# Performance work log

Hardware: AMD Instinct MI355X
Metric: run time of the kernel (lower is better)

The kernel has to match this reference:

```python
import jax, jax.numpy as jnp
import numpy as np

MAX_COC = 50.0
NUM_PLANES = 32
KERNEL_CAP = 31
B, C, H, W = 4, 3, 512, 512


def _plane_kernels():
    """Static per-plane Gaussian kernels, mirroring the torch loop exactly."""
    planes = np.linspace(0.0, MAX_COC, NUM_PLANES)
    kernels = []
    for coc in planes:
        if coc < 0.5:
            kernels.append(None)  # identity (no blur)
            continue
        sigma = coc / 2.355
        k = int(2 * coc + 1)
        if k % 2 == 0:
            k += 1
        k = min(k, KERNEL_CAP)
        coords = np.arange(k, dtype=np.float32) - k // 2
        g = np.exp(-coords ** 2 / (2.0 * sigma ** 2)).astype(np.float32)
        g = g / g.sum()
        kernels.append(np.outer(g, g).astype(np.float32))
    return planes, kernels


def _depthwise_blur(x, kern2d):
    # x: [B,C,H,W]; kern2d: [k,k] shared across channels (grouped conv, groups=C)
    c = x.shape[1]
    k = kern2d.shape[0]
    w = jnp.broadcast_to(jnp.asarray(kern2d, dtype=x.dtype)[None, None], (c, 1, k, k))
    return jax.lax.conv_general_dilated(
        x, w, window_strides=(1, 1), padding=[(k // 2, k // 2)] * 2,
        dimension_numbers=('NCHW', 'OIHW', 'NCHW'), feature_group_count=c)


def setup_inputs() -> dict:
    key = jax.random.key(0)
    k1, k2 = jax.random.split(key)
    sharp_image = jax.random.uniform(k1, (B, C, H, W), dtype=jnp.float32)
    # CoC in pixels, spanning the full [0, MAX_COC) range so all 32 bins fire
    coc_map = jax.random.uniform(k2, (B, 1, H, W), dtype=jnp.float32) * MAX_COC
    return {"sharp_image": sharp_image, "coc_map": coc_map}


def reference(sharp_image, coc_map):
    """Spatially-varying defocus blur: per-plane Gaussian blur + hard-binned blend."""
    planes, kernels = _plane_kernels()
    result = jnp.zeros_like(sharp_image)
    for i in range(NUM_PLANES):
        blurred = sharp_image if kernels[i] is None else _depthwise_blur(sharp_image, kernels[i])
        if i == 0:
            w = coc_map <= (planes[0] + planes[1]) / 2
        elif i == NUM_PLANES - 1:
            w = coc_map > (planes[-2] + planes[-1]) / 2
        else:
            lower = (planes[i - 1] + planes[i]) / 2
            upper = (planes[i] + planes[i + 1]) / 2
            w = (coc_map > lower) & (coc_map <= upper)
        # incremental masked blend (same math as stack-then-sum, less memory)
        result = result + blurred * w.astype(sharp_image.dtype)
    return result
```

## Files before the change

### kernel.cpp

```cpp
#include <hip/hip_runtime.h>
#include <math.h>

typedef _Float16 h2_t __attribute__((ext_vector_type(2)));
typedef _Float16 h4_t __attribute__((ext_vector_type(4)));
typedef _Float16 h8_t __attribute__((ext_vector_type(8)));

#define NP 32
#define KC 31
#define HH 512
#define WW 512
#define BB 4
#define CC 3

#define TXO 64
#define TYO 32
#define NT 512
#define TROWS 62
#define TWORDS 48
#define WSTR 36

__device__ h2_t g_wtabh[NP * WSTR];

__global__ void init_wtab_kernel() {
    const int tid = threadIdx.x;
    const int p = tid >> 5;
    const int t = tid & 31;
    const double stepd = 50.0 / 31.0;
    double coc = (p < 31) ? (double)p * stepd : 50.0;
    float gt;
    if (coc < 0.5) {
        gt = (t == 15) ? 1.f : 0.f;
    } else {
        double sigma = coc / 2.355;
        int k = (int)(2.0 * coc + 1.0);
        if ((k & 1) == 0) k += 1;
        if (k > KC) k = KC;
        int h = k / 2;
        int d = t - 15;
        float denom = (float)(2.0 * sigma * sigma);
        float v = (d >= -h && d <= h && t < KC) ? expf(-(float)(d * d) / denom) : 0.f;
        float s = v;
        #pragma unroll
        for (int off = 1; off < 32; off <<= 1) s += __shfl_xor(s, off, 32);
        gt = v / s;
    }
    const int m = t & 15;
    const int s0 = (t < 16) ? (2 * m) : ((2 * m - 1 < 0) ? 0 : 2 * m - 1);
    const int s1 = (t < 16) ? (2 * m + 1) : (2 * m);
    float w0 = __shfl(gt, s0, 32);
    float w1 = __shfl(gt, s1, 32);
    if (t >= 16 && (2 * m - 1) < 0) w0 = 0.f;
    h2_t w; w.x = (_Float16)w0; w.y = (_Float16)w1;
    g_wtabh[p * WSTR + t] = w;
    if (t < WSTR - 32) {
        h2_t z; z.x = (_Float16)0.f; z.y = (_Float16)0.f;
        g_wtabh[p * WSTR + 32 + t] = z;
    }
}

__device__ __forceinline__ double plane_of(int i) {
    const double stepd = 50.0 / 31.0;
    return (i < 31) ? (double)i * stepd : 50.0;
}

__launch_bounds__(512, 2)
__global__ void defocus_kernel(const float* __restrict__ img,
                               const float* __restrict__ coc,
                               float* __restrict__ out) {
    const int tx = threadIdx.x;
    const int ty = threadIdx.y;
    const int tid = ty * 16 + tx;
    const int tilex = blockIdx.x * TXO;
    const int tiley = blockIdx.y * TYO;
    const int b = blockIdx.z;

    __shared__ __align__(16) h2_t wtab[NP * WSTR];
    __shared__ __align__(16) h2_t tile[TROWS * TWORDS];

    for (int f = tid; f < NP * WSTR; f += NT) wtab[f] = g_wtabh[f];

    const int yo = tiley + ty;
    const int xo = tilex + tx * 4;

    const float4 cv = *(const float4*)&coc[((size_t)b * HH + yo) * WW + xo];
    const float cocf[4] = {cv.x, cv.y, cv.z, cv.w};
    int idx[4];
    #pragma unroll
    for (int j = 0; j < 4; ++j) {
        const double stepd = 50.0 / 31.0;
        double cd = (double)cocf[j];
        int i0 = (int)floor(cd / stepd + 0.5);
        i0 = min(max(i0, 0), 31);
        if (i0 > 0 && cd <= 0.5 * (plane_of(i0 - 1) + plane_of(i0))) {
            i0 -= 1;
        } else if (i0 < 31 && cd > 0.5 * (plane_of(i0) + plane_of(i0 + 1))) {
            i0 += 1;
        }
        idx[j] = i0;
    }

    __syncthreads();

    h2_t wj[4][16];
    #pragma unroll
    for (int j = 0; j < 4; ++j) {
        const h2_t* wp = &wtab[idx[j] * WSTR + (j & 1) * 16];
        #pragma unroll
        for (int m = 0; m < 4; ++m) {
            h8_t v = *(const h8_t*)(wp + 4 * m);
            #pragma unroll
            for (int q = 0; q < 4; ++q) {
                h2_t t; t.x = v[2 * q]; t.y = v[2 * q + 1];
                wj[j][4 * m + q] = t;
            }
        }
    }

    for (int c = 0; c < CC; ++c) {
        __syncthreads();
        const float* src = img + (size_t)(b * CC + c) * HH * WW;
        for (int f = tid; f < TROWS * TWORDS; f += NT) {
            int r = f / TWORDS;
            int w = f - r * TWORDS;
            int gy = tiley - 15 + r;
            int gx = tilex - 15 + 2 * w;
            float v0 = 0.f, v1 = 0.f;
            if ((unsigned)gy < (unsigned)HH) {
                if ((unsigned)gx < (unsigned)WW) v0 = src[gy * WW + gx];
                if ((unsigned)(gx + 1) < (unsigned)WW) v1 = src[gy * WW + gx + 1];
            }
            h2_t pv; pv.x = (_Float16)v0; pv.y = (_Float16)v1;
            tile[f] = pv;
        }
        __syncthreads();

        float acc0 = 0.f, acc1 = 0.f, acc2 = 0.f, acc3 = 0.f;
        const h2_t* rowbase = &tile[ty * TWORDS + 2 * tx];
        #pragma unroll
        for (int dy = 0; dy < KC; ++dy) {
            const h2_t* rp = rowbase + dy * TWORDS;
            h2_t rw[18];
            #pragma unroll
            for (int m = 0; m < 9; ++m) {
                h4_t q = *(const h4_t*)(rp + 2 * m);
                h2_t lo; lo.x = q[0]; lo.y = q[1];
                h2_t hi; hi.x = q[2]; hi.y = q[3];
                rw[2 * m]     = lo;
                rw[2 * m + 1] = hi;
            }
            float rs0 = 0.f, rs1 = 0.f, rs2 = 0.f, rs3 = 0.f;
            #pragma unroll
            for (int m = 0; m < 16; ++m) {
                rs0 = __builtin_amdgcn_fdot2(wj[0][m], rw[m],     rs0, false);
                rs1 = __builtin_amdgcn_fdot2(wj[1][m], rw[m],     rs1, false);
                rs2 = __builtin_amdgcn_fdot2(wj[2][m], rw[m + 1], rs2, false);
                rs3 = __builtin_amdgcn_fdot2(wj[3][m], rw[m + 1], rs3, false);
            }
            float cw0, cw1, cw2, cw3;
            if ((dy & 1) == 0) {
                cw0 = (float)wj[0][dy >> 1].x;
                cw2 = (float)wj[2][dy >> 1].x;
                cw1 = (float)wj[1][dy >> 1].y;
                cw3 = (float)wj[3][dy >> 1].y;
            } else {
                cw0 = (float)wj[0][dy >> 1].y;
                cw2 = (float)wj[2][dy >> 1].y;
                cw1 = (float)wj[1][(dy + 1) >> 1].x;
                cw3 = (float)wj[3][(dy + 1) >> 1].x;
            }
            acc0 += cw0 * rs0;
            acc1 += cw1 * rs1;
            acc2 += cw2 * rs2;
            acc3 += cw3 * rs3;
        }

        *(float4*)&out[((size_t)(b * CC + c) * HH + yo) * WW + xo] =
            make_float4(acc0, acc1, acc2, acc3);
    }
}

extern "C" void kernel_launch(void* const* d_in, const int* in_sizes, int n_in,
                              void* d_out, int out_size, void* d_ws, size_t ws_size,
                              hipStream_t stream) {
    const float* sharp = (const float*)d_in[0];
    const float* cocm  = (const float*)d_in[1];
    float* out = (float*)d_out;

    init_wtab_kernel<<<1, 1024, 0, stream>>>();
    dim3 grid(WW / TXO, HH / TYO, BB);
    dim3 block(16, 32, 1);
    defocus_kernel<<<grid, block, 0, stream>>>(sharp, cocm, out);
}
```

Baseline: 136.3 us.

## Preload all channel tiles into LDS, stagger channel order, split dot chains

All three channel tiles are now staged into shared memory once, before the single existing barrier. This removes the per-channel load and sync phases that used to serialize global loads with compute. Each wave starts on a different channel, which spreads LDS read traffic, and each fdot2 accumulation is split into two independent chains for more instruction-level parallelism. Shared memory per block roughly triples, which may limit occupancy, and the split changes the fp summation order.

Result: slower. 160.5 us (+17.8%).

```diff
diff --git a/kernel.cpp b/kernel.cpp
--- a/kernel.cpp
+++ b/kernel.cpp
@@ -17,6 +17,7 @@
 #define NT 512
 #define TROWS 62
 #define TWORDS 48
+#define TILEW (TROWS * TWORDS)
 #define WSTR 36
 
 __device__ h2_t g_wtabh[NP * WSTR];
@@ -75,9 +76,28 @@
     const int b = blockIdx.z;
 
     __shared__ __align__(16) h2_t wtab[NP * WSTR];
-    __shared__ __align__(16) h2_t tile[TROWS * TWORDS];
+    __shared__ __align__(16) h2_t tiles[CC * TILEW];
 
     for (int f = tid; f < NP * WSTR; f += NT) wtab[f] = g_wtabh[f];
+
+    #pragma unroll
+    for (int c = 0; c < CC; ++c) {
+        const float* src = img + (size_t)(b * CC + c) * HH * WW;
+        h2_t* tc = &tiles[c * TILEW];
+        for (int f = tid; f < TILEW; f += NT) {
+            int r = f / TWORDS;
+            int w = f - r * TWORDS;
+            int gy = tiley - 15 + r;
+            int gx = tilex - 15 + 2 * w;
+            float v0 = 0.f, v1 = 0.f;
+            if ((unsigned)gy < (unsigned)HH) {
+                if ((unsigned)gx < (unsigned)WW) v0 = src[gy * WW + gx];
+                if ((unsigned)(gx + 1) < (unsigned)WW) v1 = src[gy * WW + gx + 1];
+            }
+            h2_t pv; pv.x = (_Float16)v0; pv.y = (_Float16)v1;
+            tc[f] = pv;
+        }
+    }
 
     const int yo = tiley + ty;
     const int xo = tilex + tx * 4;
@@ -116,26 +136,12 @@
         }
     }
 
-    for (int c = 0; c < CC; ++c) {
-        __syncthreads();
-        const float* src = img + (size_t)(b * CC + c) * HH * WW;
-        for (int f = tid; f < TROWS * TWORDS; f += NT) {
-            int r = f / TWORDS;
-            int w = f - r * TWORDS;
-            int gy = tiley - 15 + r;
-            int gx = tilex - 15 + 2 * w;
-            float v0 = 0.f, v1 = 0.f;
-            if ((unsigned)gy < (unsigned)HH) {
-                if ((unsigned)gx < (unsigned)WW) v0 = src[gy * WW + gx];
-                if ((unsigned)(gx + 1) < (unsigned)WW) v1 = src[gy * WW + gx + 1];
-            }
-            h2_t pv; pv.x = (_Float16)v0; pv.y = (_Float16)v1;
-            tile[f] = pv;
-        }
-        __syncthreads();
-
+    const int c0 = (tid >> 6) % 3;
+
+    for (int cc = 0; cc < CC; ++cc) {
+        int c = c0 + cc; if (c >= CC) c -= CC;
         float acc0 = 0.f, acc1 = 0.f, acc2 = 0.f, acc3 = 0.f;
-        const h2_t* rowbase = &tile[ty * TWORDS + 2 * tx];
+        const h2_t* rowbase = &tiles[c * TILEW + ty * TWORDS + 2 * tx];
         #pragma unroll
         for (int dy = 0; dy < KC; ++dy) {
             const h2_t* rp = rowbase + dy * TWORDS;
@@ -148,14 +154,23 @@
                 rw[2 * m]     = lo;
                 rw[2 * m + 1] = hi;
             }
-            float rs0 = 0.f, rs1 = 0.f, rs2 = 0.f, rs3 = 0.f;
+            float ra0 = 0.f, rb0 = 0.f, ra1 = 0.f, rb1 = 0.f;
+            float ra2 = 0.f, rb2 = 0.f, ra3 = 0.f, rb3 = 0.f;
             #pragma unroll
-            for (int m = 0; m < 16; ++m) {
-                rs0 = __builtin_amdgcn_fdot2(wj[0][m], rw[m],     rs0, false);
-                rs1 = __builtin_amdgcn_fdot2(wj[1][m], rw[m],     rs1, false);
-                rs2 = __builtin_amdgcn_fdot2(wj[2][m], rw[m + 1], rs2, false);
-                rs3 = __builtin_amdgcn_fdot2(wj[3][m], rw[m + 1], rs3, false);
-            }
+            for (int m = 0; m < 8; ++m) {
+                ra0 = __builtin_amdgcn_fdot2(wj[0][m],     rw[m],     ra0, false);
+                rb0 = __builtin_amdgcn_fdot2(wj[0][m + 8], rw[m + 8], rb0, false);
+                ra1 = __builtin_amdgcn_fdot2(wj[1][m],     rw[m],     ra1, false);
+                rb1 = __builtin_amdgcn_fdot2(wj[1][m + 8], rw[m + 8], rb1, false);
+                ra2 = __builtin_amdgcn_fdot2(wj[2][m],     rw[m + 1], ra2, false);
+                rb2 = __builtin_amdgcn_fdot2(wj[2][m + 8], rw[m + 9], rb2, false);
+                ra3 = __builtin_amdgcn_fdot2(wj[3][m],     rw[m + 1], ra3, false);
+                rb3 = __builtin_amdgcn_fdot2(wj[3][m + 8], rw[m + 9], rb3, false);
+            }
+            float rs0 = ra0 + rb0;
+            float rs1 = ra1 + rb1;
+            float rs2 = ra2 + rb2;
+            float rs3 = ra3 + rb3;
             float cw0, cw1, cw2, cw3;
             if ((dy & 1) == 0) {
                 cw0 = (float)wj[0][dy >> 1].x;
```
